# Optimization experiments

Measured on AMD Instinct MI355X. Metric: run time of the kernel, lower is better.

## Reference

```python
import math
import jax, jax.numpy as jnp
import numpy as np

N_HEADS = 8
FACTOR = 1


def setup_inputs() -> dict:
    key = jax.random.key(0)
    ks = jax.random.split(key, 8)
    B, L, D = 8, 2048, 512
    scale = 0.05
    return {
        "queries": jax.random.normal(ks[0], (B, L, D), jnp.float32),
        "keys": jax.random.normal(ks[1], (B, L, D), jnp.float32),
        "values": jax.random.normal(ks[2], (B, L, D), jnp.float32),
        "Wq": jax.random.normal(ks[3], (D, D), jnp.float32) * scale,
        "bq": jnp.zeros((D,), jnp.float32),
        "Wk": jax.random.normal(ks[4], (D, D), jnp.float32) * scale,
        "bk": jnp.zeros((D,), jnp.float32),
        "Wv": jax.random.normal(ks[5], (D, D), jnp.float32) * scale,
        "bv": jnp.zeros((D,), jnp.float32),
        "Wo": jax.random.normal(ks[6], (D, D), jnp.float32) * scale,
        "bo": jnp.zeros((D,), jnp.float32),
    }


def _autocorrelation(q, k, v):
    # q,k,v: [B, L, H, E]; L == S assumed (as built in setup_inputs)
    B, L, H, E = q.shape
    qp = jnp.transpose(q, (0, 2, 3, 1))  # [B,H,E,L]
    kp = jnp.transpose(k, (0, 2, 3, 1))
    vp = jnp.transpose(v, (0, 2, 3, 1))
    q_fft = jnp.fft.rfft(qp, axis=-1)
    k_fft = jnp.fft.rfft(kp, axis=-1)
    corr = jnp.fft.irfft(q_fft * jnp.conj(k_fft), n=L, axis=-1)  # [B,H,E,L]

    # training-path time-delay aggregation
    top_k = int(FACTOR * math.log(L))  # static python int
    mean_value = corr.mean(axis=(1, 2))  # [B, L]
    _, index = jax.lax.top_k(mean_value.mean(axis=0), top_k)  # [K] global delays
    weights = mean_value[:, index]  # [B, K]
    tmp_corr = jax.nn.softmax(weights, axis=-1)  # [B, K]
    # roll(v, -d) along last axis == gather at (t + d) mod L
    idx = (jnp.arange(L)[None, :] + index[:, None]) % L  # [K, L]
    patterns = vp[..., idx]  # [B,H,E,K,L]
    delays_agg = jnp.einsum('bhekl,bk->bhel', patterns, tmp_corr)  # [B,H,E,L]
    return jnp.transpose(delays_agg, (0, 3, 1, 2))  # [B,L,H,E]


def reference(queries, keys, values, Wq, bq, Wk, bk, Wv, bv, Wo, bo):
    B, L, Dm = queries.shape
    H = N_HEADS
    q = (queries @ Wq + bq).reshape(B, L, H, -1)
    k = (keys @ Wk + bk).reshape(B, L, H, -1)
    v = (values @ Wv + bv).reshape(B, L, H, -1)
    out = _autocorrelation(q, k, v).reshape(B, L, -1)
    return out @ Wo + bo
```

## Files before the change

kernel.cpp:

```cpp
#include <hip/hip_runtime.h>
#include <stdint.h>

#define BATCH 8
#define L_SEQ 2048
#define D_MODEL 512
#define TOPK 7
#define BM 128
#define BN 128
#define BK 32
#define LT 136

typedef _Float16 f16x8 __attribute__((ext_vector_type(8)));
typedef __attribute__((ext_vector_type(4))) float f32x4;
typedef unsigned short u16;
typedef unsigned int u32;

__device__ __forceinline__ u16 f2h(float f) {
    union { _Float16 h; u16 u; } v; v.h = (_Float16)f; return v.u;
}

__device__ __forceinline__ void load_lds16(const u16* g, u16* l) {
    __builtin_amdgcn_global_load_lds(
        (const __attribute__((address_space(1))) u32*)(g),
        (__attribute__((address_space(3))) u32*)(l), 16, 0, 0);
}


__global__ __launch_bounds__(256, 3) void gemm_qkv(
    const float* __restrict__ Xq, const float* __restrict__ Xk, const float* __restrict__ Xv,
    const u16* __restrict__ Wqt, const u16* __restrict__ Wkt, const u16* __restrict__ Wvt,
    const float* __restrict__ bq, const float* __restrict__ bk, const float* __restrict__ bv,
    u16* __restrict__ QT, u16* __restrict__ KT, u16* __restrict__ Vout)
{
    __shared__ __align__(16) u16 smem[2 * BM * 32 + 2 * BN * BK];
    u16* lT = smem;
    u16* lBb = smem + 2 * BM * 32;

    const int tid = threadIdx.x;
    const int hw = blockIdx.x;
    const int lg = (hw & 7) * 192 + (hw >> 3);
    const int bn = lg & 3, bm = (lg >> 2) & 127, z = lg >> 9;

    const int lane = tid & 63, wave = tid >> 6;
    const int wm = wave >> 1, wn = wave & 1;
    const int l15 = lane & 15, quad = lane >> 4;

    const float* A  = (z == 0) ? Xq  : (z == 1) ? Xk  : Xv;
    const u16*   Bt = (z == 0) ? Wqt : (z == 1) ? Wkt : Wvt;
    const float* bias = (z == 0) ? bq : (z == 1) ? bk : bv;

    const int s0 = wave * 64 + lane, s1 = s0 + 256;
    const int r0 = s0 >> 2, c0 = (s0 & 3) ^ ((r0 >> 1) & 3);
    const int r1 = s1 >> 2, c1 = (s1 & 3) ^ ((r1 >> 1) & 3);
    const u16* gB0 = Bt + (long)(bn * BN + r0) * D_MODEL + c0 * 8;
    const u16* gB1 = Bt + (long)(bn * BN + r1) * D_MODEL + c1 * 8;

    f32x4 acc[4][4] = {};

    {
        load_lds16(gB0, lBb + wave * 512);
        load_lds16(gB1, lBb + 2048 + wave * 512);
        gB0 += BK; gB1 += BK;
        #pragma unroll
        for (int j = 0; j < 4; ++j) {
            int idx = tid + j * 256;
            int row = idx >> 3, c4 = (idx & 7) * 4;
            int cs = (((c4 >> 3) ^ (row & 3)) << 3) | (c4 & 7);
            float4 va = *(const float4*)(A + (long)(bm * BM + row) * D_MODEL + c4);
            ushort4 pa;
            pa.x = f2h(va.x); pa.y = f2h(va.y); pa.z = f2h(va.z); pa.w = f2h(va.w);
            *(ushort4*)&smem[row * 32 + cs] = pa;
        }
    }
    __syncthreads();

    for (int t = 0; t < 16; ++t) {
        const int cur = t & 1;
        u16* lAc = smem + cur * (BM * 32);
        u16* lBc = lBb + cur * (BN * BK);
        u16* lAn = smem + (cur ^ 1) * (BM * 32);
        u16* lBn = lBb + (cur ^ 1) * (BN * BK);
        const bool nx = (t < 15);
        const int k1 = (t + 1) * BK;

        float4 va[4];
        if (nx) {
            load_lds16(gB0, lBn + wave * 512);
            load_lds16(gB1, lBn + 2048 + wave * 512);
            gB0 += BK; gB1 += BK;
            #pragma unroll
            for (int j = 0; j < 4; ++j) {
                int idx = tid + j * 256;
                int row = idx >> 3, c4 = (idx & 7) * 4;
                va[j] = *(const float4*)(A + (long)(bm * BM + row) * D_MODEL + k1 + c4);
            }
        }

        f16x8 fa[4], fb[4];
        #pragma unroll
        for (int i = 0; i < 4; ++i) {
            int r = wm * 64 + i * 16 + l15;
            fa[i] = *(const f16x8*)&lAc[r * 32 + ((quad ^ (r & 3)) << 3)];
        }
        #pragma unroll
        for (int j = 0; j < 4; ++j) {
            int n = wn * 64 + j * 16 + l15;
            int cs = quad ^ ((n >> 1) & 3);
            fb[j] = *(const f16x8*)&lBc[n * 32 + cs * 8];
        }
        #pragma unroll
        for (int i = 0; i < 4; ++i)
            #pragma unroll
            for (int j = 0; j < 4; ++j)
                acc[i][j] = __builtin_amdgcn_mfma_f32_16x16x32_f16(fa[i], fb[j], acc[i][j], 0, 0, 0);

        if (nx) {
            #pragma unroll
            for (int j = 0; j < 4; ++j) {
                int idx = tid + j * 256;
                int row = idx >> 3, c4 = (idx & 7) * 4;
                int cs = (((c4 >> 3) ^ (row & 3)) << 3) | (c4 & 7);
                ushort4 pa;
                pa.x = f2h(va[j].x); pa.y = f2h(va[j].y);
                pa.z = f2h(va[j].z); pa.w = f2h(va[j].w);
                *(ushort4*)&lAn[row * 32 + cs] = pa;
            }
        }
        __syncthreads();
    }

    if (z < 2) {
        u16* out = (z == 0) ? QT : KT;
        const int t0 = (bm * BM) & (L_SEQ - 1);
        const int bb = (bm * BM) >> 11;
        #pragma unroll
        for (int h = 0; h < 2; ++h) {
            __syncthreads();
            if (wn == h) {
                #pragma unroll
                for (int j = 0; j < 4; ++j) {
                    int dloc = j * 16 + l15;
                    float bvv = bias[bn * BN + h * 64 + dloc];
                    #pragma unroll
                    for (int i = 0; i < 4; ++i) {
                        int trow = wm * 64 + i * 16 + quad * 4;
                        #pragma unroll
                        for (int r = 0; r < 4; ++r)
                            lT[dloc * LT + trow + r] = f2h(acc[i][j][r] + bvv);
                    }
                }
            }
            __syncthreads();
            int dloc = tid >> 2, q4 = tid & 3;
            long base = ((long)(bb * D_MODEL + bn * BN + h * 64 + dloc)) * L_SEQ + t0;
            #pragma unroll
            for (int s = 0; s < 4; ++s) {
                int c = q4 * 4 + s;
                *(uint4*)(out + base + c * 8) = *(const uint4*)&lT[dloc * LT + c * 8];
            }
        }
    } else {
        #pragma unroll
        for (int i = 0; i < 4; ++i) {
            int row = bm * BM + wm * 64 + i * 16 + quad * 4;
            #pragma unroll
            for (int j = 0; j < 4; ++j) {
                int col = bn * BN + wn * 64 + j * 16 + l15;
                float bvv = bias[col];
                #pragma unroll
                for (int r = 0; r < 4; ++r)
                    Vout[(long)(row + r) * D_MODEL + col] = f2h(acc[i][j][r] + bvv);
            }
        }
    }
}

__global__ __launch_bounds__(256, 3) void gemm_out_fused(
    const u16* __restrict__ V, const u16* __restrict__ Bt,
    const int* __restrict__ selIdx, const float* __restrict__ selW,
    const float* __restrict__ bias, float* __restrict__ Cp)
{
    __shared__ __align__(16) u16 lA[2 * BM * 32];
    __shared__ __align__(16) u16 lB[2 * BN * BK];

    const int tid = threadIdx.x;
    const int hw = blockIdx.x;
    const int lg = (hw & 7) * 64 + (hw >> 3);
    const int bn = lg & 3, bm = lg >> 2;

    const int lane = tid & 63, wave = tid >> 6;
    const int wm = wave >> 1, wn = wave & 1;
    const int l15 = lane & 15, quad = lane >> 4;

    int sik[TOPK];
    #pragma unroll
    for (int k = 0; k < TOPK; ++k) sik[k] = selIdx[k];

    const int s0 = wave * 64 + lane, s1 = s0 + 256;
    const int r0 = s0 >> 2, c0 = (s0 & 3) ^ ((r0 >> 1) & 3);
    const int r1 = s1 >> 2, c1 = (s1 & 3) ^ ((r1 >> 1) & 3);
    const u16* gB0 = Bt + (long)(bn * BN + r0) * D_MODEL + c0 * 8;
    const u16* gB1 = Bt + (long)(bn * BN + r1) * D_MODEL + c1 * 8;

    const int row_a = tid >> 2,          c8_a = (tid & 3) * 8;
    const int row_b = (tid + 256) >> 2,  c8_b = (tid & 3) * 8;
    const int csa = ((c8_a >> 3) ^ (row_a & 3)) << 3;
    const int csb = ((c8_b >> 3) ^ (row_b & 3)) << 3;
    const int gra = bm * BM + row_a, grb = bm * BM + row_b;
    const int ba = gra >> 11, la = gra & (L_SEQ - 1);
    const int bb = grb >> 11, lb = grb & (L_SEQ - 1);

    _Float16 swa[TOPK], swb[TOPK];
    #pragma unroll
    for (int k = 0; k < TOPK; ++k) {
        swa[k] = (_Float16)selW[ba * TOPK + k];
        swb[k] = (_Float16)selW[bb * TOPK + k];
    }

    union U8 { uint4 u; f16x8 h8; };

    f32x4 acc[4][4] = {};

    {
        load_lds16(gB0, lB + wave * 512);
        load_lds16(gB1, lB + 2048 + wave * 512);
        gB0 += BK; gB1 += BK;
        {
            f16x8 a = {};
            #pragma unroll
            for (int k = 0; k < TOPK; ++k) {
                int src = (la + sik[k]) & (L_SEQ - 1);
                U8 x; x.u = *(const uint4*)(V + ((long)ba * L_SEQ + src) * D_MODEL + c8_a);
                a += x.h8 * swa[k];
            }
            U8 o; o.h8 = a;
            *(uint4*)&lA[row_a * 32 + csa] = o.u;
        }
        {
            f16x8 a = {};
            #pragma unroll
            for (int k = 0; k < TOPK; ++k) {
                int src = (lb + sik[k]) & (L_SEQ - 1);
                U8 x; x.u = *(const uint4*)(V + ((long)bb * L_SEQ + src) * D_MODEL + c8_b);
                a += x.h8 * swb[k];
            }
            U8 o; o.h8 = a;
            *(uint4*)&lA[row_b * 32 + csb] = o.u;
        }
    }
    __syncthreads();

    for (int t = 0; t < 16; ++t) {
        const int cur = t & 1;
        u16* lAc = lA + cur * (BM * 32);
        u16* lBc = lB + cur * (BN * BK);
        u16* lAn = lA + (cur ^ 1) * (BM * 32);
        u16* lBn = lB + (cur ^ 1) * (BN * BK);
        const bool nx = (t < 15);
        const int k1 = (t + 1) * BK;

        U8 xv[7];
        if (nx) {
            load_lds16(gB0, lBn + wave * 512);
            load_lds16(gB1, lBn + 2048 + wave * 512);
            gB0 += BK; gB1 += BK;
            #pragma unroll
            for (int k = 0; k < TOPK; ++k) {
                int src = (la + sik[k]) & (L_SEQ - 1);
                xv[k].u = *(const uint4*)(V + ((long)ba * L_SEQ + src) * D_MODEL + k1 + c8_a);
            }
        }

        f16x8 fa[4], fb[4];
        #pragma unroll
        for (int i = 0; i < 4; ++i) {
            int r = wm * 64 + i * 16 + l15;
            fa[i] = *(const f16x8*)&lAc[r * 32 + ((quad ^ (r & 3)) << 3)];
        }
        #pragma unroll
        for (int j = 0; j < 4; ++j) {
            int n = wn * 64 + j * 16 + l15;
            int cs = quad ^ ((n >> 1) & 3);
            fb[j] = *(const f16x8*)&lBc[n * 32 + cs * 8];
        }

        #pragma unroll
        for (int i = 0; i < 2; ++i)
            #pragma unroll
            for (int j = 0; j < 4; ++j)
                acc[i][j] = __builtin_amdgcn_mfma_f32_16x16x32_f16(fa[i], fb[j], acc[i][j], 0, 0, 0);

        U8 xw[7];
        if (nx) {
            f16x8 a = {};
            #pragma unroll
            for (int k = 0; k < TOPK; ++k) a += xv[k].h8 * swa[k];
            U8 o; o.h8 = a;
            *(uint4*)&lAn[row_a * 32 + csa] = o.u;
            #pragma unroll
            for (int k = 0; k < TOPK; ++k) {
                int src = (lb + sik[k]) & (L_SEQ - 1);
                xw[k].u = *(const uint4*)(V + ((long)bb * L_SEQ + src) * D_MODEL + k1 + c8_b);
            }
        }

        #pragma unroll
        for (int i = 2; i < 4; ++i)
            #pragma unroll
            for (int j = 0; j < 4; ++j)
                acc[i][j] = __builtin_amdgcn_mfma_f32_16x16x32_f16(fa[i], fb[j], acc[i][j], 0, 0, 0);

        if (nx) {
            f16x8 a = {};
            #pragma unroll
            for (int k = 0; k < TOPK; ++k) a += xw[k].h8 * swb[k];
            U8 o; o.h8 = a;
            *(uint4*)&lAn[row_b * 32 + csb] = o.u;
        }
        __syncthreads();
    }

    #pragma unroll
    for (int i = 0; i < 4; ++i) {
        int row = bm * BM + wm * 64 + i * 16 + quad * 4;
        #pragma unroll
        for (int j = 0; j < 4; ++j) {
            int col = bn * BN + wn * 64 + j * 16 + l15;
            float bvv = bias[col];
            #pragma unroll
            for (int r = 0; r < 4; ++r)
                Cp[(long)(row + r) * D_MODEL + col] = acc[i][j][r] + bvv;
        }
    }
}

__device__ __forceinline__ void fft2048_lds(
    float* Zr, float* Zi, const float* Twr, const float* Twi, int tid)
{
    #pragma unroll
    for (int s = 0; s < 10; s += 2) {
        #pragma unroll
        for (int u = 0; u < 2; ++u) {
            int idx = tid + u * 256;
            int d1 = 1 << s;
            int pos = idx & (d1 - 1);
            int i0 = ((idx >> s) << (s + 2)) + pos;
            float w1r = Twr[pos << (10 - s)], w1i = Twi[pos << (10 - s)];
            float w2r = Twr[pos << (9 - s)],  w2i = Twi[pos << (9 - s)];
            int p2 = pos + d1;
            float w3r = Twr[p2 << (9 - s)],   w3i = Twi[p2 << (9 - s)];
            float ar = Zr[i0],          ai = Zi[i0];
            float br = Zr[i0 + d1],     bi = Zi[i0 + d1];
            float cr = Zr[i0 + 2 * d1], ci = Zi[i0 + 2 * d1];
            float dr = Zr[i0 + 3 * d1], di = Zi[i0 + 3 * d1];
            float t1r = br * w1r - bi * w1i, t1i = br * w1i + bi * w1r;
            float Ar = ar + t1r, Ai = ai + t1i, Br = ar - t1r, Bi = ai - t1i;
            float t2r = dr * w1r - di * w1i, t2i = dr * w1i + di * w1r;
            float Cr = cr + t2r, Ci = ci + t2i, Dr = cr - t2r, Di = ci - t2i;
            float u1r = Cr * w2r - Ci * w2i, u1i = Cr * w2i + Ci * w2r;
            float u2r = Dr * w3r - Di * w3i, u2i = Dr * w3i + Di * w3r;
            Zr[i0]          = Ar + u1r; Zi[i0]          = Ai + u1i;
            Zr[i0 + 2 * d1] = Ar - u1r; Zi[i0 + 2 * d1] = Ai - u1i;
            Zr[i0 + d1]     = Br + u2r; Zi[i0 + d1]     = Bi + u2i;
            Zr[i0 + 3 * d1] = Br - u2r; Zi[i0 + 3 * d1] = Bi - u2i;
        }
        __syncthreads();
    }
    #pragma unroll
    for (int j = 0; j < 4; ++j) {
        int idx = tid + j * 256;
        float wr = Twr[idx], wi = Twi[idx];
        float ar = Zr[idx], ai = Zi[idx];
        float br = Zr[idx + 1024], bi = Zi[idx + 1024];
        float tr = br * wr - bi * wi, ti = br * wi + bi * wr;
        Zr[idx] = ar + tr; Zi[idx] = ai + ti;
        Zr[idx + 1024] = ar - tr; Zi[idx + 1024] = ai - ti;
    }
    __syncthreads();
}

__global__ __launch_bounds__(256) void fft_corr_fwd(
    const u16* __restrict__ QT, const u16* __restrict__ KT, float* __restrict__ P)
{
    __shared__ float Zr[2048], Zi[2048];
    __shared__ float Twr[1024], Twi[1024];
    const int tid = threadIdx.x;
    const int b = blockIdx.x >> 7, dg = blockIdx.x & 127;

    #pragma unroll
    for (int j = 0; j < 4; ++j) {
        int i = tid + j * 256;
        float ang = -6.28318530717958647692f * (float)i * (1.0f / 2048.0f);
        float sn, cs; __sincosf(ang, &sn, &cs);
        Twr[i] = cs; Twi[i] = sn;
    }

    float sr[8] = {0,0,0,0,0,0,0,0};
    float si8[8] = {0,0,0,0,0,0,0,0};

    for (int g = 0; g < 4; ++g) {
        int d = dg * 4 + g;
        const u16* qrow = QT + ((long)b * D_MODEL + d) * L_SEQ;
        const u16* krow = KT + ((long)b * D_MODEL + d) * L_SEQ;
        __syncthreads();
        union { uint4 u; _Float16 h[8]; } xq, xk;
        xq.u = *(const uint4*)(qrow + tid * 8);
        xk.u = *(const uint4*)(krow + tid * 8);
        #pragma unroll
        for (int j = 0; j < 8; ++j) {
            int t = tid * 8 + j;
            int tr = (int)(__brev((unsigned)t) >> 21);
            Zr[tr] = (float)xq.h[j];
            Zi[tr] = (float)xk.h[j];
        }
        __syncthreads();
        fft2048_lds(Zr, Zi, Twr, Twi, tid);
        #pragma unroll
        for (int j = 0; j < 8; ++j) {
            int f = tid + j * 256;
            int fm = (2048 - f) & 2047;
            float Xr = Zr[f], Xi = Zi[f], Xmr = Zr[fm], Xmi = Zi[fm];
            float qr = 0.5f * (Xr + Xmr), qi = 0.5f * (Xi - Xmi);
            float dr = Xr - Xmr,          di = Xi + Xmi;
            float kr = 0.5f * di,         ki = -0.5f * dr;
            sr[j]  += qr * kr + qi * ki;
            si8[j] += qi * kr - qr * ki;
        }
    }
    float* Pb = P + ((long)(b * 128 + dg) * 2048) * 2;
    #pragma unroll
    for (int j = 0; j < 8; ++j) {
        int f = tid + j * 256;
        float2 v; v.x = sr[j]; v.y = si8[j];
        *(float2*)(Pb + (long)f * 2) = v;
    }
}

__global__ __launch_bounds__(256) void fft_reduce(
    const float* __restrict__ P, float* __restrict__ S)
{
    const int b = blockIdx.x >> 3, fc = blockIdx.x & 7;
    const int f = fc * 256 + threadIdx.x;
    const float* base = P + ((long)b * 128 * 2048 + f) * 2;
    float sr = 0.f, si = 0.f;
    for (int dg = 0; dg < 128; ++dg) {
        float2 v = *(const float2*)(base + (long)dg * 4096);
        sr += v.x; si += v.y;
    }
    float2 o; o.x = sr; o.y = si;
    *(float2*)(S + ((long)b * 2048 + f) * 2) = o;
}

__global__ __launch_bounds__(256) void fft_corr_inv(
    const float* __restrict__ S, float* __restrict__ raw)
{
    __shared__ float Zr[2048], Zi[2048];
    __shared__ float Twr[1024], Twi[1024];
    const int tid = threadIdx.x;
    const int b = blockIdx.x;

    #pragma unroll
    for (int j = 0; j < 4; ++j) {
        int i = tid + j * 256;
        float ang = 6.28318530717958647692f * (float)i * (1.0f / 2048.0f);
        float sn, cs; __sincosf(ang, &sn, &cs);
        Twr[i] = cs; Twi[i] = sn;
    }
    #pragma unroll
    for (int j = 0; j < 8; ++j) {
        int f = tid + j * 256;
        int fr = (int)(__brev((unsigned)f) >> 21);
        Zr[fr] = S[((long)b * 2048 + f) * 2 + 0];
        Zi[fr] = S[((long)b * 2048 + f) * 2 + 1];
    }
    __syncthreads();
    fft2048_lds(Zr, Zi, Twr, Twi, tid);
    #pragma unroll
    for (int j = 0; j < 8; ++j) {
        int t = tid + j * 256;
        raw[(long)b * 2048 + t] = Zr[t] * (1.0f / 2048.0f);
    }
}

__global__ __launch_bounds__(256) void transposeW4(
    const float* __restrict__ Wq, const float* __restrict__ Wk,
    const float* __restrict__ Wv, const float* __restrict__ Wo, u16* __restrict__ dstBase)
{
    __shared__ float t[32][33];
    const int z = blockIdx.z;
    const float* src = (z == 0) ? Wq : (z == 1) ? Wk : (z == 2) ? Wv : Wo;
    u16* dst = dstBase + (long)z * D_MODEL * D_MODEL;
    int tx = threadIdx.x & 31, ty = threadIdx.x >> 5;
    int c0 = blockIdx.x * 32, r0 = blockIdx.y * 32;
    #pragma unroll
    for (int r = ty; r < 32; r += 8)
        t[r][tx] = src[(long)(r0 + r) * D_MODEL + c0 + tx];
    __syncthreads();
    #pragma unroll
    for (int r = ty; r < 32; r += 8)
        dst[(long)(c0 + r) * D_MODEL + r0 + tx] = f2h(t[tx][r]);
}

__global__ __launch_bounds__(256) void select_topk(
    const float* __restrict__ raw, int* __restrict__ selIdx, float* __restrict__ selW)
{
    __shared__ float g[L_SEQ];
    __shared__ float wv[4];
    __shared__ int   wi[4];
    __shared__ int   sidx[TOPK];
    __shared__ float wbuf[BATCH][TOPK];
    int tid = threadIdx.x;
    int lane = tid & 63, wave = tid >> 6;
    for (int t = tid; t < L_SEQ; t += 256) {
        float s = 0.0f;
        #pragma unroll
        for (int b = 0; b < BATCH; ++b) s += raw[b * L_SEQ + t];
        g[t] = s;
    }
    __syncthreads();
    for (int it = 0; it < TOPK; ++it) {
        float best = -1e30f; int bi = 0x7fffffff;
        #pragma unroll
        for (int j = 0; j < 8; ++j) {
            int t = tid + j * 256;
            float v = g[t];
            if (v > best || (v == best && t < bi)) { best = v; bi = t; }
        }
        #pragma unroll
        for (int s = 32; s > 0; s >>= 1) {
            float v2 = __shfl_xor(best, s);
            int   i2 = __shfl_xor(bi, s);
            if (v2 > best || (v2 == best && i2 < bi)) { best = v2; bi = i2; }
        }
        if (lane == 0) { wv[wave] = best; wi[wave] = bi; }
        __syncthreads();
        if (tid == 0) {
            float b0 = wv[0]; int i0 = wi[0];
            #pragma unroll
            for (int w = 1; w < 4; ++w)
                if (wv[w] > b0 || (wv[w] == b0 && wi[w] < i0)) { b0 = wv[w]; i0 = wi[w]; }
            sidx[it] = i0; g[i0] = -1e30f;
        }
        __syncthreads();
    }
    if (tid < BATCH * TOPK) {
        int b = tid / TOPK, k = tid % TOPK;
        wbuf[b][k] = raw[b * L_SEQ + sidx[k]] * (1.0f / 512.0f);
    }
    __syncthreads();
    if (tid < BATCH) {
        float mx = -1e30f;
        #pragma unroll
        for (int k = 0; k < TOPK; ++k) mx = fmaxf(mx, wbuf[tid][k]);
        float e[TOPK]; float sum = 0.0f;
        #pragma unroll
        for (int k = 0; k < TOPK; ++k) { e[k] = expf(wbuf[tid][k] - mx); sum += e[k]; }
        #pragma unroll
        for (int k = 0; k < TOPK; ++k) selW[tid * TOPK + k] = e[k] / sum;
    }
    if (tid < TOPK) selIdx[tid] = sidx[tid];
}

extern "C" void kernel_launch(void* const* d_in, const int* in_sizes, int n_in,
                              void* d_out, int out_size, void* d_ws, size_t ws_size,
                              hipStream_t stream)
{
    (void)in_sizes; (void)n_in; (void)out_size; (void)ws_size;
    const float* Xq = (const float*)d_in[0];
    const float* Xk = (const float*)d_in[1];
    const float* Xv = (const float*)d_in[2];
    const float* Wq = (const float*)d_in[3];
    const float* bq = (const float*)d_in[4];
    const float* Wk = (const float*)d_in[5];
    const float* bk = (const float*)d_in[6];
    const float* Wv = (const float*)d_in[7];
    const float* bv = (const float*)d_in[8];
    const float* Wo = (const float*)d_in[9];
    const float* bo = (const float*)d_in[10];

    char* ws = (char*)d_ws;
    const long SLABH = (long)BATCH * L_SEQ * D_MODEL * sizeof(u16);
    u16* QT   = (u16*)(ws);
    u16* KT   = (u16*)(ws + SLABH);
    u16* Vf   = (u16*)(ws + 2 * SLABH);
    const long WSZ = (long)D_MODEL * D_MODEL;
    u16* Wt   = (u16*)(ws + 3 * SLABH);
    u16* Wqt = Wt + 0 * WSZ; u16* Wkt = Wt + 1 * WSZ;
    u16* Wvt = Wt + 2 * WSZ; u16* Wot = Wt + 3 * WSZ;
    float* S   = (float*)(ws + 3 * SLABH + 4 * WSZ * sizeof(u16));
    float* raw = S + (long)BATCH * L_SEQ * 2;
    int*   sIdx = (int*)(raw + (long)BATCH * L_SEQ);
    float* sW   = (float*)(sIdx + 8);
    float* P    = (float*)(sW + 64);

    dim3 tb(256);
    transposeW4<<<dim3(16, 16, 4), tb, 0, stream>>>(Wq, Wk, Wv, Wo, Wt);

    gemm_qkv<<<dim3(1536), tb, 0, stream>>>(Xq, Xk, Xv, Wqt, Wkt, Wvt, bq, bk, bv, QT, KT, Vf);

    fft_corr_fwd<<<dim3(1024), tb, 0, stream>>>(QT, KT, P);
    fft_reduce<<<dim3(64), tb, 0, stream>>>(P, S);
    fft_corr_inv<<<dim3(BATCH), tb, 0, stream>>>(S, raw);
    select_topk<<<1, tb, 0, stream>>>(raw, sIdx, sW);

    gemm_out_fused<<<dim3(512), tb, 0, stream>>>(Vf, Wot, sIdx, sW, bo, (float*)d_out);
}
```

Baseline: 309.5 us.

## Deepen QKV GEMM prefetch pipeline and parallelize FFT partial reduction

```diff
diff --git a/kernel.cpp b/kernel.cpp
--- a/kernel.cpp
+++ b/kernel.cpp
@@ -55,7 +55,19 @@
     const u16* gB0 = Bt + (long)(bn * BN + r0) * D_MODEL + c0 * 8;
     const u16* gB1 = Bt + (long)(bn * BN + r1) * D_MODEL + c1 * 8;
 
+    int rowj[4], csj[4];
+    const float* gA[4];
+    #pragma unroll
+    for (int j = 0; j < 4; ++j) {
+        int idx = tid + j * 256;
+        int row = idx >> 3, c4 = (idx & 7) * 4;
+        rowj[j] = row;
+        csj[j] = (((c4 >> 3) ^ (row & 3)) << 3) | (c4 & 7);
+        gA[j] = A + (long)(bm * BM + row) * D_MODEL + c4;
+    }
+
     f32x4 acc[4][4] = {};
+    float4 vaA[4];
 
     {
         load_lds16(gB0, lBb + wave * 512);
@@ -63,71 +75,100 @@
         gB0 += BK; gB1 += BK;
         #pragma unroll
         for (int j = 0; j < 4; ++j) {
-            int idx = tid + j * 256;
-            int row = idx >> 3, c4 = (idx & 7) * 4;
-            int cs = (((c4 >> 3) ^ (row & 3)) << 3) | (c4 & 7);
-            float4 va = *(const float4*)(A + (long)(bm * BM + row) * D_MODEL + c4);
+            float4 va = *(const float4*)(gA[j]);
             ushort4 pa;
             pa.x = f2h(va.x); pa.y = f2h(va.y); pa.z = f2h(va.z); pa.w = f2h(va.w);
-            *(ushort4*)&smem[row * 32 + cs] = pa;
-        }
-    }
-    __syncthreads();
-
-    for (int t = 0; t < 16; ++t) {
+            *(ushort4*)&smem[rowj[j] * 32 + csj[j]] = pa;
+        }
+        #pragma unroll
+        for (int j = 0; j < 4; ++j)
+            vaA[j] = *(const float4*)(gA[j] + BK);
+    }
+    __syncthreads();
+
+    #define QKV_FRAGS_MFMA(lAc_, lBc_)                                              \
+        {                                                                           \
+            f16x8 fa[4], fb[4];                                                     \
+            _Pragma("unroll")                                                       \
+            for (int i = 0; i < 4; ++i) {                                           \
+                int r = wm * 64 + i * 16 + l15;                                     \
+                fa[i] = *(const f16x8*)&(lAc_)[r * 32 + ((quad ^ (r & 3)) << 3)];   \
+            }                                                                       \
+            _Pragma("unroll")                                                       \
+            for (int j = 0; j < 4; ++j) {                                           \
+                int n = wn * 64 + j * 16 + l15;                                     \
+                int cs = quad ^ ((n >> 1) & 3);                                     \
+                fb[j] = *(const f16x8*)&(lBc_)[n * 32 + cs * 8];                    \
+            }                                                                       \
+            _Pragma("unroll")                                                       \
+            for (int i = 0; i < 4; ++i)                                             \
+                _Pragma("unroll")                                                   \
+                for (int j = 0; j < 4; ++j)                                         \
+                    acc[i][j] = __builtin_amdgcn_mfma_f32_16x16x32_f16(             \
+                        fa[i], fb[j], acc[i][j], 0, 0, 0);                          \
+        }
+
+    for (int t = 0; t < 14; ++t) {
         const int cur = t & 1;
         u16* lAc = smem + cur * (BM * 32);
         u16* lBc = lBb + cur * (BN * BK);
         u16* lAn = smem + (cur ^ 1) * (BM * 32);
         u16* lBn = lBb + (cur ^ 1) * (BN * BK);
-        const bool nx = (t < 15);
-        const int k1 = (t + 1) * BK;
-
-        float4 va[4];
-        if (nx) {
-            load_lds16(gB0, lBn + wave * 512);
-            load_lds16(gB1, lBn + 2048 + wave * 512);
-            gB0 += BK; gB1 += BK;
-            #pragma unroll
-            for (int j = 0; j < 4; ++j) {
-                int idx = tid + j * 256;
-                int row = idx >> 3, c4 = (idx & 7) * 4;
-                va[j] = *(const float4*)(A + (long)(bm * BM + row) * D_MODEL + k1 + c4);
-            }
-        }
-
-        f16x8 fa[4], fb[4];
-        #pragma unroll
-        for (int i = 0; i < 4; ++i) {
-            int r = wm * 64 + i * 16 + l15;
-            fa[i] = *(const f16x8*)&lAc[r * 32 + ((quad ^ (r & 3)) << 3)];
-        }
+
         #pragma unroll
         for (int j = 0; j < 4; ++j) {
-            int n = wn * 64 + j * 16 + l15;
-            int cs = quad ^ ((n >> 1) & 3);
-            fb[j] = *(const f16x8*)&lBc[n * 32 + cs * 8];
-        }
-        #pragma unroll
-        for (int i = 0; i < 4; ++i)
-            #pragma unroll
-            for (int j = 0; j < 4; ++j)
-                acc[i][j] = __builtin_amdgcn_mfma_f32_16x16x32_f16(fa[i], fb[j], acc[i][j], 0, 0, 0);
-
-        if (nx) {
-            #pragma unroll
-            for (int j = 0; j < 4; ++j) {
-                int idx = tid + j * 256;
-                int row = idx >> 3, c4 = (idx & 7) * 4;
-                int cs = (((c4 >> 3) ^ (row & 3)) << 3) | (c4 & 7);
-                ushort4 pa;
-                pa.x = f2h(va[j].x); pa.y = f2h(va[j].y);
-                pa.z = f2h(va[j].z); pa.w = f2h(va[j].w);
-                *(ushort4*)&lAn[row * 32 + cs] = pa;
-            }
-        }
-        __syncthreads();
-    }
+            ushort4 pa;
+            pa.x = f2h(vaA[j].x); pa.y = f2h(vaA[j].y);
+            pa.z = f2h(vaA[j].z); pa.w = f2h(vaA[j].w);
+            *(ushort4*)&lAn[rowj[j] * 32 + csj[j]] = pa;
+        }
+        __builtin_amdgcn_sched_barrier(0);
+        load_lds16(gB0, lBn + wave * 512);
+        load_lds16(gB1, lBn + 2048 + wave * 512);
+        gB0 += BK; gB1 += BK;
+        __builtin_amdgcn_sched_barrier(0);
+        #pragma unroll
+        for (int j = 0; j < 4; ++j)
+            vaA[j] = *(const float4*)(gA[j] + (t + 2) * BK);
+
+        QKV_FRAGS_MFMA(lAc, lBc)
+
+        asm volatile("s_waitcnt vmcnt(4) lgkmcnt(0)" ::: "memory");
+        __builtin_amdgcn_sched_barrier(0);
+        __builtin_amdgcn_s_barrier();
+        __builtin_amdgcn_sched_barrier(0);
+    }
+
+    {
+        u16* lAc = smem;
+        u16* lBc = lBb;
+        u16* lAn = smem + BM * 32;
+        u16* lBn = lBb + BN * BK;
+        #pragma unroll
+        for (int j = 0; j < 4; ++j) {
+            ushort4 pa;
+            pa.x = f2h(vaA[j].x); pa.y = f2h(vaA[j].y);
+            pa.z = f2h(vaA[j].z); pa.w = f2h(vaA[j].w);
+            *(ushort4*)&lAn[rowj[j] * 32 + csj[j]] = pa;
+        }
+        __builtin_amdgcn_sched_barrier(0);
+        load_lds16(gB0, lBn + wave * 512);
+        load_lds16(gB1, lBn + 2048 + wave * 512);
+
+        QKV_FRAGS_MFMA(lAc, lBc)
+
+        asm volatile("s_waitcnt vmcnt(0) lgkmcnt(0)" ::: "memory");
+        __builtin_amdgcn_sched_barrier(0);
+        __builtin_amdgcn_s_barrier();
+        __builtin_amdgcn_sched_barrier(0);
+    }
+
+    {
+        u16* lAc = smem + BM * 32;
+        u16* lBc = lBb + BN * BK;
+        QKV_FRAGS_MFMA(lAc, lBc)
+    }
+    #undef QKV_FRAGS_MFMA
 
     if (z < 2) {
         u16* out = (z == 0) ? QT : KT;
@@ -439,16 +480,26 @@
 __global__ __launch_bounds__(256) void fft_reduce(
     const float* __restrict__ P, float* __restrict__ S)
 {
-    const int b = blockIdx.x >> 3, fc = blockIdx.x & 7;
-    const int f = fc * 256 + threadIdx.x;
+    __shared__ float red[2][4][64];
+    const int blk = blockIdx.x;
+    const int b = blk >> 5, fc = blk & 31;
+    const int q = threadIdx.x >> 6, fl = threadIdx.x & 63;
+    const int f = fc * 64 + fl;
     const float* base = P + ((long)b * 128 * 2048 + f) * 2;
     float sr = 0.f, si = 0.f;
-    for (int dg = 0; dg < 128; ++dg) {
-        float2 v = *(const float2*)(base + (long)dg * 4096);
+    #pragma unroll 4
+    for (int d = q * 32; d < q * 32 + 32; ++d) {
+        float2 v = *(const float2*)(base + (long)d * 4096);
         sr += v.x; si += v.y;
     }
-    float2 o; o.x = sr; o.y = si;
-    *(float2*)(S + ((long)b * 2048 + f) * 2) = o;
+    red[0][q][fl] = sr; red[1][q][fl] = si;
+    __syncthreads();
+    if (q == 0) {
+        float osr = red[0][0][fl] + red[0][1][fl] + red[0][2][fl] + red[0][3][fl];
+        float osi = red[1][0][fl] + red[1][1][fl] + red[1][2][fl] + red[1][3][fl];
+        float2 o; o.x = osr; o.y = osi;
+        *(float2*)(S + ((long)b * 2048 + f) * 2) = o;
+    }
 }
 
 __global__ __launch_bounds__(256) void fft_corr_inv(
@@ -599,7 +650,7 @@
     gemm_qkv<<<dim3(1536), tb, 0, stream>>>(Xq, Xk, Xv, Wqt, Wkt, Wvt, bq, bk, bv, QT, KT, Vf);
 
     fft_corr_fwd<<<dim3(1024), tb, 0, stream>>>(QT, KT, P);
-    fft_reduce<<<dim3(64), tb, 0, stream>>>(P, S);
+    fft_reduce<<<dim3(256), tb, 0, stream>>>(P, S);
     fft_corr_inv<<<dim3(BATCH), tb, 0, stream>>>(S, raw);
     select_topk<<<1, tb, 0, stream>>>(raw, sIdx, sW);
 
```

After: 308.4 us. Within noise of the previous version (-0.3%).
